# Optimization experiments

Measured on AMD Instinct MI355X. Metric: run time of the kernel, lower is better.

## Reference

```python
import jax, jax.numpy as jnp
import numpy as np


def setup_inputs() -> dict:
    key = jax.random.key(0)
    ks = jax.random.split(key, 7)
    B, C, W, H = 4, 256, 128, 128
    s = 1.0 / np.sqrt(C)
    return {
        "x": jax.random.normal(ks[0], (B, C, W, H), dtype=jnp.float32),
        "wq": jax.random.normal(ks[1], (C, C), dtype=jnp.float32) * s,
        "bq": jax.random.normal(ks[2], (C,), dtype=jnp.float32) * s,
        "wk": jax.random.normal(ks[3], (C, C), dtype=jnp.float32) * s,
        "bk": jax.random.normal(ks[4], (C,), dtype=jnp.float32) * s,
        "wv": jax.random.normal(ks[5], (C, C), dtype=jnp.float32) * s,
        "bv": jax.random.normal(ks[6], (C,), dtype=jnp.float32) * s,
    }


def reference(x, wq, bq, wk, bk, wv, bv):
    B, C, W, H = x.shape
    N = W * H
    xf = x.reshape(B, C, N)  # flatten spatial: (B, C, N)
    # 1x1 convs are channel-mixing GEMMs: out[b,o,n] = sum_c w[o,c] x[b,c,n] + b[o]
    q = jnp.einsum('oc,bcn->bon', wq, xf) + bq[:, None]
    k = jnp.einsum('oc,bcn->bon', wk, xf) + bk[:, None]
    v = jnp.einsum('oc,bcn->bon', wv, xf) + bv[:, None]
    # channel-channel energy: (B, C, C)
    energy = jnp.einsum('bcn,bdn->bcd', q, k) / jnp.sqrt(jnp.float32(N))
    attention = jax.nn.softmax(energy, axis=-1)
    out = jnp.einsum('bcd,bdn->bcn', attention, v)
    return out.reshape(B, C, W, H) + x
```

## Files before the change

kernel.cpp:

```cpp
#include <hip/hip_runtime.h>
#include <stdint.h>

#define BB 4
#define CC 256
#define NN 16384
#define NSL 32

typedef unsigned short u16;
typedef __attribute__((ext_vector_type(8))) __bf16 bf16x8;
typedef __attribute__((ext_vector_type(4))) float f32x4;

__device__ __forceinline__ u16 f2bf(float f) {
  union { float f; uint32_t u; } c;
  c.f = f;
  uint32_t u = c.u;
  return (u16)((u + 0x7fffu + ((u >> 16) & 1u)) >> 16);
}

__device__ __forceinline__ void g2l16(const u16* g, u16* l) {
  __builtin_amdgcn_global_load_lds((__attribute__((address_space(1))) void*)g,
                                   (__attribute__((address_space(3))) void*)l, 16, 0, 0);
}

__device__ __forceinline__ void stage128x32(const u16* src, int stride, u16* lds, int tid) {
  int r = tid >> 2;
  int c = (tid & 3) << 3;
  g2l16(src + (size_t)r * stride + c, lds + r * 32 + c);
  g2l16(src + (size_t)(r + 64) * stride + c, lds + (r + 64) * 32 + c);
}

__device__ __forceinline__ void stage128x32_w8(const u16* src, int stride, u16* lds, int tid) {
  int r = tid >> 2;
  int c = (tid & 3) << 3;
  g2l16(src + (size_t)r * stride + c, lds + r * 32 + c);
}

__device__ __forceinline__ void stage256x32_w8(const u16* src, int stride, u16* lds, int tid) {
  int r = tid >> 2;
  int c = (tid & 3) << 3;
  g2l16(src + (size_t)r * stride + c, lds + r * 32 + c);
  g2l16(src + (size_t)(r + 128) * stride + c, lds + (r + 128) * 32 + c);
}

__device__ __forceinline__ void mfma_tile(const u16* As, const u16* Bs, int mb, int nb,
                                          int l16, int q8, f32x4 acc[4][4]) {
  bf16x8 af[4], bf[4];
#pragma unroll
  for (int i = 0; i < 4; i++) af[i] = *(const bf16x8*)&As[(mb + i * 16 + l16) * 32 + q8];
#pragma unroll
  for (int i = 0; i < 4; i++) bf[i] = *(const bf16x8*)&Bs[(nb + i * 16 + l16) * 32 + q8];
#pragma unroll
  for (int i = 0; i < 4; i++)
#pragma unroll
    for (int j = 0; j < 4; j++)
      acc[i][j] = __builtin_amdgcn_mfma_f32_16x16x32_bf16(af[i], bf[j], acc[i][j], 0, 0, 0);
}

__global__ __launch_bounds__(256) void prep_kernel(const float* __restrict__ x,
                                                   u16* __restrict__ xb,
                                                   u16* __restrict__ xbT,
                                                   float* __restrict__ s_part) {
  __shared__ float t[64][65];
  __shared__ float rs[64][4];
  int n0 = blockIdx.x * 64, c0 = blockIdx.y * 64, bz = blockIdx.z;
  int tid = threadIdx.x;
  int rr0 = tid >> 4, q4 = (tid & 15) * 4;
  const float* xs = x + ((size_t)bz * CC + c0) * NN + n0;
  u16* xbp = xb + ((size_t)bz * CC + c0) * NN + n0;
#pragma unroll
  for (int cc = rr0; cc < 64; cc += 16) {
    float4 v = *(const float4*)&xs[(size_t)cc * NN + q4];
    t[cc][q4] = v.x; t[cc][q4 + 1] = v.y; t[cc][q4 + 2] = v.z; t[cc][q4 + 3] = v.w;
    union { u16 h[4]; uint2 u; } pk;
    pk.h[0] = f2bf(v.x); pk.h[1] = f2bf(v.y); pk.h[2] = f2bf(v.z); pk.h[3] = f2bf(v.w);
    *(uint2*)&xbp[(size_t)cc * NN + q4] = pk.u;
  }
  __syncthreads();
  {
    int r = tid >> 2, q = tid & 3;
    float p = 0.f;
#pragma unroll
    for (int i = 0; i < 16; i++) p += t[r][q * 16 + i];
    rs[r][q] = p;
  }
  u16* od = xbT + ((size_t)bz * NN + n0) * CC + c0;
#pragma unroll
  for (int nn = rr0; nn < 64; nn += 16) {
    union { u16 h[4]; uint2 u; } pk;
    pk.h[0] = f2bf(t[q4][nn]); pk.h[1] = f2bf(t[q4 + 1][nn]);
    pk.h[2] = f2bf(t[q4 + 2][nn]); pk.h[3] = f2bf(t[q4 + 3][nn]);
    *(uint2*)&od[(size_t)nn * CC + q4] = pk.u;
  }
  __syncthreads();
  if (tid < 64)
    s_part[((size_t)bz * 256 + blockIdx.x) * CC + c0 + tid] =
        rs[tid][0] + rs[tid][1] + rs[tid][2] + rs[tid][3];
}

__global__ __launch_bounds__(256) void gram_kernel(const u16* __restrict__ xb,
                                                   float* __restrict__ Gp) {
  __shared__ u16 As[2][128 * 32], Bs[2][128 * 32];
  int tid = threadIdx.x;
  int c0 = (blockIdx.x >> 1) * 128, d0 = (blockIdx.x & 1) * 128;
  int sl = blockIdx.y, bz = blockIdx.z;
  const u16* A = xb + ((size_t)bz * CC + c0) * NN + sl * 512;
  const u16* Bt = xb + ((size_t)bz * CC + d0) * NN + sl * 512;
  f32x4 acc[4][4] = {};
  int wave = tid >> 6, lane = tid & 63;
  int mb = (wave >> 1) * 64, nb = (wave & 1) * 64;
  int quad = lane >> 4, l16 = lane & 15, q8 = quad * 8;
  for (int kk = 0; kk < 512; kk += 64) {
    stage128x32(A + kk, NN, As[0], tid);
    stage128x32(A + kk + 32, NN, As[1], tid);
    stage128x32(Bt + kk, NN, Bs[0], tid);
    stage128x32(Bt + kk + 32, NN, Bs[1], tid);
    __syncthreads();
    mfma_tile(As[0], Bs[0], mb, nb, l16, q8, acc);
    mfma_tile(As[1], Bs[1], mb, nb, l16, q8, acc);
    __syncthreads();
  }
  float* gp = Gp + ((size_t)sl * BB + bz) * CC * CC;
#pragma unroll
  for (int i = 0; i < 4; i++)
#pragma unroll
    for (int j = 0; j < 4; j++)
#pragma unroll
      for (int r = 0; r < 4; r++)
        gp[(size_t)(c0 + mb + i * 16 + quad * 4 + r) * CC + d0 + nb + j * 16 + l16] =
            acc[i][j][r];
}

__global__ __launch_bounds__(256) void reduce_kernel(const float* __restrict__ Gp,
                                                     const float* __restrict__ s_part,
                                                     const float* __restrict__ Wk,
                                                     float* __restrict__ G,
                                                     float* __restrict__ s,
                                                     float* __restrict__ WkT) {
  __shared__ float tw[32][33];
  int t = threadIdx.x, blk = blockIdx.x;
  size_t base = ((size_t)blk * 256 + t) * 4;
  float ax = 0.f, ay = 0.f, az = 0.f, aw = 0.f;
#pragma unroll 8
  for (int sl = 0; sl < NSL; sl++) {
    float4 v = *(const float4*)&Gp[(size_t)sl * (BB * CC * CC) + base];
    ax += v.x; ay += v.y; az += v.z; aw += v.w;
  }
  float4 o; o.x = ax; o.y = ay; o.z = az; o.w = aw;
  *(float4*)&G[base] = o;
  if (blk < BB) {
    float a = 0.f;
#pragma unroll 8
    for (int nt = 0; nt < 256; nt++) a += s_part[((size_t)blk * 256 + nt) * CC + t];
    s[blk * CC + t] = a;
  }
  if (blk < 64) {
    int tr = blk >> 3, tc = blk & 7;
    int r = t >> 5, c = t & 31;
#pragma unroll
    for (int i = 0; i < 4; i++)
      tw[r + i * 8][c] = Wk[(size_t)(tr * 32 + r + i * 8) * CC + tc * 32 + c];
    __syncthreads();
#pragma unroll
    for (int i = 0; i < 4; i++)
      WkT[(size_t)(tc * 32 + r + i * 8) * CC + tr * 32 + c] = tw[c][r + i * 8];
  }
}

__global__ __launch_bounds__(256) void mid_kernel(
    const float* __restrict__ G, const float* __restrict__ s,
    const float* __restrict__ Wq, const float* __restrict__ WkT,
    const float* __restrict__ Wv,
    const float* __restrict__ bq, const float* __restrict__ bk,
    const float* __restrict__ bv,
    u16* __restrict__ Mvb, float* __restrict__ bo) {
  __shared__ float sS[CC];
  __shared__ float rS[2][CC];
  __shared__ float attS[2][CC];
  __shared__ float redA[2][4], redB[2][4], redC[2][4], redD[2][4];
  int t = threadIdx.x;
  int o0 = blockIdx.x * 2, b = blockIdx.y;
  int wv = t >> 6, ln = t & 63;
  sS[t] = s[b * CC + t];
  __syncthreads();
  float p0 = Wq[(size_t)o0 * CC + t] * sS[t];
  float p1 = Wq[(size_t)(o0 + 1) * CC + t] * sS[t];
#pragma unroll
  for (int d = 32; d > 0; d >>= 1) {
    p0 += __shfl_xor(p0, d, 64);
    p1 += __shfl_xor(p1, d, 64);
  }
  if (ln == 0) { redA[0][wv] = p0; redA[1][wv] = p1; }
  __syncthreads();
  float up0 = redA[0][0] + redA[0][1] + redA[0][2] + redA[0][3] + 16384.f * bq[o0];
  float up1 = redA[1][0] + redA[1][1] + redA[1][2] + redA[1][3] + 16384.f * bq[o0 + 1];
  const float* Gb = G + (size_t)b * CC * CC;
  const float* wq0 = Wq + (size_t)o0 * CC;
  const float* wq1 = wq0 + CC;
  float r0 = bq[o0] * sS[t], r1 = bq[o0 + 1] * sS[t];
#pragma unroll 8
  for (int d = 0; d < CC; d++) {
    float g = Gb[d * CC + t];
    r0 += wq0[d] * g;
    r1 += wq1[d] * g;
  }
  rS[0][t] = r0;
  rS[1][t] = r1;
  __syncthreads();
  float e0 = up0 * bk[t], e1 = up1 * bk[t];
#pragma unroll 8
  for (int c = 0; c < CC; c++) {
    float w = WkT[(size_t)c * CC + t];
    e0 += rS[0][c] * w;
    e1 += rS[1][c] * w;
  }
  e0 *= 0.0078125f;
  e1 *= 0.0078125f;
  float m0 = e0, m1 = e1;
#pragma unroll
  for (int d = 32; d > 0; d >>= 1) {
    m0 = fmaxf(m0, __shfl_xor(m0, d, 64));
    m1 = fmaxf(m1, __shfl_xor(m1, d, 64));
  }
  if (ln == 0) { redB[0][wv] = m0; redB[1][wv] = m1; }
  __syncthreads();
  m0 = fmaxf(fmaxf(redB[0][0], redB[0][1]), fmaxf(redB[0][2], redB[0][3]));
  m1 = fmaxf(fmaxf(redB[1][0], redB[1][1]), fmaxf(redB[1][2], redB[1][3]));
  e0 = __expf(e0 - m0);
  e1 = __expf(e1 - m1);
  float s0 = e0, s1 = e1;
#pragma unroll
  for (int d = 32; d > 0; d >>= 1) {
    s0 += __shfl_xor(s0, d, 64);
    s1 += __shfl_xor(s1, d, 64);
  }
  if (ln == 0) { redC[0][wv] = s0; redC[1][wv] = s1; }
  __syncthreads();
  float inv0 = 1.f / (redC[0][0] + redC[0][1] + redC[0][2] + redC[0][3]);
  float inv1 = 1.f / (redC[1][0] + redC[1][1] + redC[1][2] + redC[1][3]);
  float a0 = e0 * inv0, a1 = e1 * inv1;
  attS[0][t] = a0;
  attS[1][t] = a1;
  float b0 = a0 * bv[t], b1 = a1 * bv[t];
#pragma unroll
  for (int d = 32; d > 0; d >>= 1) {
    b0 += __shfl_xor(b0, d, 64);
    b1 += __shfl_xor(b1, d, 64);
  }
  if (ln == 0) { redD[0][wv] = b0; redD[1][wv] = b1; }
  __syncthreads();
  if (t == 0) bo[b * CC + o0] = redD[0][0] + redD[0][1] + redD[0][2] + redD[0][3];
  if (t == 1) bo[b * CC + o0 + 1] = redD[1][0] + redD[1][1] + redD[1][2] + redD[1][3];
  float mv0 = 0.f, mv1 = 0.f;
#pragma unroll 8
  for (int d = 0; d < CC; d++) {
    float w = Wv[d * CC + t];
    mv0 += attS[0][d] * w;
    mv1 += attS[1][d] * w;
  }
  Mvb[((size_t)b * CC + o0) * CC + t] = f2bf(mv0);
  Mvb[((size_t)b * CC + o0 + 1) * CC + t] = f2bf(mv1);
}

__global__ __launch_bounds__(512) void out_kernel(const u16* __restrict__ Mvb,
                                                  const u16* __restrict__ xbT,
                                                  const float* __restrict__ bo,
                                                  const float* __restrict__ x,
                                                  float* __restrict__ out) {
  __shared__ u16 As[2][128 * 32], Bs[2][256 * 32];
  int tid = threadIdx.x;
  int n0 = blockIdx.x * 256, m0 = blockIdx.y * 128, bz = blockIdx.z;
  const u16* A = Mvb + (size_t)bz * CC * CC + (size_t)m0 * CC;
  const u16* Bt = xbT + ((size_t)bz * NN + n0) * CC;
  f32x4 acc[4][4] = {};
  int wave = tid >> 6, lane = tid & 63;
  int mb = (wave & 1) * 64, nb = (wave >> 1) * 64;
  int quad = lane >> 4, l16 = lane & 15, q8 = quad * 8;
  for (int kk = 0; kk < CC; kk += 64) {
    stage128x32_w8(A + kk, CC, As[0], tid);
    stage128x32_w8(A + kk + 32, CC, As[1], tid);
    stage256x32_w8(Bt + kk, CC, Bs[0], tid);
    stage256x32_w8(Bt + kk + 32, CC, Bs[1], tid);
    __syncthreads();
    mfma_tile(As[0], Bs[0], mb, nb, l16, q8, acc);
    mfma_tile(As[1], Bs[1], mb, nb, l16, q8, acc);
    __syncthreads();
  }
#pragma unroll
  for (int i = 0; i < 4; i++)
#pragma unroll
    for (int r = 0; r < 4; r++) {
      int cg = m0 + mb + i * 16 + quad * 4 + r;
      float bc = bo[bz * CC + cg];
#pragma unroll
      for (int j = 0; j < 4; j++) {
        int ng = n0 + nb + j * 16 + l16;
        size_t idx = ((size_t)bz * CC + cg) * NN + ng;
        out[idx] = acc[i][j][r] + bc + x[idx];
      }
    }
}

extern "C" void kernel_launch(void* const* d_in, const int* in_sizes, int n_in,
                              void* d_out, int out_size, void* d_ws, size_t ws_size,
                              hipStream_t stream) {
  (void)in_sizes; (void)n_in; (void)out_size; (void)ws_size;
  const float* x = (const float*)d_in[0];
  const float* wq = (const float*)d_in[1];
  const float* bq = (const float*)d_in[2];
  const float* wk = (const float*)d_in[3];
  const float* bk = (const float*)d_in[4];
  const float* wv = (const float*)d_in[5];
  const float* bv = (const float*)d_in[6];
  float* out = (float*)d_out;

  char* ws = (char*)d_ws;
  u16* xb      = (u16*)(ws + 0);
  u16* xbT     = (u16*)(ws + 33554432);
  float* Gp    = (float*)(ws + 67108864);
  float* G     = (float*)(ws + 100663296);
  float* s_prt = (float*)(ws + 101711872);
  float* s     = (float*)(ws + 102760448);
  u16* Mvb     = (u16*)(ws + 102764544);
  float* bo    = (float*)(ws + 103288832);
  float* WkT   = (float*)(ws + 103292928);

  prep_kernel<<<dim3(NN / 64, CC / 64, BB), 256, 0, stream>>>(x, xb, xbT, s_prt);
  gram_kernel<<<dim3(4, NSL, BB), 256, 0, stream>>>(xb, Gp);
  reduce_kernel<<<256, 256, 0, stream>>>(Gp, s_prt, wk, G, s, WkT);
  mid_kernel<<<dim3(CC / 2, BB), 256, 0, stream>>>(G, s, wq, WkT, wv, bq, bk, bv, Mvb, bo);
  out_kernel<<<dim3(NN / 256, CC / 128, BB), 512, 0, stream>>>(Mvb, xbT, bo, x, out);
}
```

Baseline: 233.6 us.

## Restructure mid_kernel for 4 rows per block and vectorize out_kernel epilogue via LDS

```diff
diff --git a/kernel.cpp b/kernel.cpp
--- a/kernel.cpp
+++ b/kernel.cpp
@@ -166,7 +166,7 @@
   }
 }
 
-__global__ __launch_bounds__(256) void mid_kernel(
+__global__ __launch_bounds__(512) void mid_kernel(
     const float* __restrict__ G, const float* __restrict__ s,
     const float* __restrict__ Wq, const float* __restrict__ WkT,
     const float* __restrict__ Wv,
@@ -174,91 +174,136 @@
     const float* __restrict__ bv,
     u16* __restrict__ Mvb, float* __restrict__ bo) {
   __shared__ float sS[CC];
-  __shared__ float rS[2][CC];
-  __shared__ float attS[2][CC];
-  __shared__ float redA[2][4], redB[2][4], redC[2][4], redD[2][4];
+  __shared__ float wqS[4][CC];
+  __shared__ float rS[4][CC];
+  __shared__ float attS[4][CC];
+  __shared__ float part[4][8][CC];
+  __shared__ float redA[4][4], redB[4][4], redC[4][4], redD[4][4];
   int t = threadIdx.x;
-  int o0 = blockIdx.x * 2, b = blockIdx.y;
+  int o0 = blockIdx.x * 4, b = blockIdx.y;
   int wv = t >> 6, ln = t & 63;
-  sS[t] = s[b * CC + t];
-  __syncthreads();
-  float p0 = Wq[(size_t)o0 * CC + t] * sS[t];
-  float p1 = Wq[(size_t)(o0 + 1) * CC + t] * sS[t];
+  int col = t & 255;
+  int row_a = t >> 8, row_b = row_a + 2;
+  int c4 = ln << 2;
+  int d0 = wv << 5;
+  if (t < CC) sS[t] = s[b * CC + t];
+  {
+    const float* wqsrc = Wq + (size_t)o0 * CC;
+    ((float*)wqS)[t] = wqsrc[t];
+    ((float*)wqS)[t + 512] = wqsrc[t + 512];
+  }
+  __syncthreads();
+  float pa = wqS[row_a][col] * sS[col];
+  float pb = wqS[row_b][col] * sS[col];
 #pragma unroll
   for (int d = 32; d > 0; d >>= 1) {
-    p0 += __shfl_xor(p0, d, 64);
-    p1 += __shfl_xor(p1, d, 64);
-  }
-  if (ln == 0) { redA[0][wv] = p0; redA[1][wv] = p1; }
-  __syncthreads();
-  float up0 = redA[0][0] + redA[0][1] + redA[0][2] + redA[0][3] + 16384.f * bq[o0];
-  float up1 = redA[1][0] + redA[1][1] + redA[1][2] + redA[1][3] + 16384.f * bq[o0 + 1];
+    pa += __shfl_xor(pa, d, 64);
+    pb += __shfl_xor(pb, d, 64);
+  }
+  if (ln == 0) { redA[row_a][wv & 3] = pa; redA[row_b][wv & 3] = pb; }
+  __syncthreads();
+  float up_a = redA[row_a][0] + redA[row_a][1] + redA[row_a][2] + redA[row_a][3] +
+               16384.f * bq[o0 + row_a];
+  float up_b = redA[row_b][0] + redA[row_b][1] + redA[row_b][2] + redA[row_b][3] +
+               16384.f * bq[o0 + row_b];
   const float* Gb = G + (size_t)b * CC * CC;
-  const float* wq0 = Wq + (size_t)o0 * CC;
-  const float* wq1 = wq0 + CC;
-  float r0 = bq[o0] * sS[t], r1 = bq[o0 + 1] * sS[t];
-#pragma unroll 8
-  for (int d = 0; d < CC; d++) {
-    float g = Gb[d * CC + t];
-    r0 += wq0[d] * g;
-    r1 += wq1[d] * g;
-  }
-  rS[0][t] = r0;
-  rS[1][t] = r1;
-  __syncthreads();
-  float e0 = up0 * bk[t], e1 = up1 * bk[t];
-#pragma unroll 8
-  for (int c = 0; c < CC; c++) {
-    float w = WkT[(size_t)c * CC + t];
-    e0 += rS[0][c] * w;
-    e1 += rS[1][c] * w;
-  }
-  e0 *= 0.0078125f;
-  e1 *= 0.0078125f;
-  float m0 = e0, m1 = e1;
+  {
+    f32x4 va[4] = {};
+    const float* gp = Gb + (size_t)d0 * CC + c4;
+#pragma unroll 8
+    for (int i = 0; i < 32; i++) {
+      f32x4 g4 = *(const f32x4*)(gp + (size_t)i * CC);
+      float w0 = wqS[0][d0 + i], w1 = wqS[1][d0 + i];
+      float w2 = wqS[2][d0 + i], w3 = wqS[3][d0 + i];
+      va[0] += g4 * w0; va[1] += g4 * w1; va[2] += g4 * w2; va[3] += g4 * w3;
+    }
+#pragma unroll
+    for (int r = 0; r < 4; r++) *(f32x4*)&part[r][wv][c4] = va[r];
+  }
+  __syncthreads();
+  {
+    float r_a = bq[o0 + row_a] * sS[col];
+    float r_b = bq[o0 + row_b] * sS[col];
+#pragma unroll
+    for (int w = 0; w < 8; w++) { r_a += part[row_a][w][col]; r_b += part[row_b][w][col]; }
+    rS[row_a][col] = r_a;
+    rS[row_b][col] = r_b;
+  }
+  __syncthreads();
+  {
+    f32x4 ve[4] = {};
+    const float* wkp = WkT + (size_t)d0 * CC + c4;
+#pragma unroll 8
+    for (int i = 0; i < 32; i++) {
+      f32x4 w4 = *(const f32x4*)(wkp + (size_t)i * CC);
+      float r0 = rS[0][d0 + i], r1 = rS[1][d0 + i];
+      float r2 = rS[2][d0 + i], r3 = rS[3][d0 + i];
+      ve[0] += w4 * r0; ve[1] += w4 * r1; ve[2] += w4 * r2; ve[3] += w4 * r3;
+    }
+#pragma unroll
+    for (int r = 0; r < 4; r++) *(f32x4*)&part[r][wv][c4] = ve[r];
+  }
+  __syncthreads();
+  float bkc = bk[col];
+  float e_a = up_a * bkc, e_b = up_b * bkc;
+#pragma unroll
+  for (int w = 0; w < 8; w++) { e_a += part[row_a][w][col]; e_b += part[row_b][w][col]; }
+  e_a *= 0.0078125f;
+  e_b *= 0.0078125f;
+  float m_a = e_a, m_b = e_b;
 #pragma unroll
   for (int d = 32; d > 0; d >>= 1) {
-    m0 = fmaxf(m0, __shfl_xor(m0, d, 64));
-    m1 = fmaxf(m1, __shfl_xor(m1, d, 64));
-  }
-  if (ln == 0) { redB[0][wv] = m0; redB[1][wv] = m1; }
-  __syncthreads();
-  m0 = fmaxf(fmaxf(redB[0][0], redB[0][1]), fmaxf(redB[0][2], redB[0][3]));
-  m1 = fmaxf(fmaxf(redB[1][0], redB[1][1]), fmaxf(redB[1][2], redB[1][3]));
-  e0 = __expf(e0 - m0);
-  e1 = __expf(e1 - m1);
-  float s0 = e0, s1 = e1;
+    m_a = fmaxf(m_a, __shfl_xor(m_a, d, 64));
+    m_b = fmaxf(m_b, __shfl_xor(m_b, d, 64));
+  }
+  if (ln == 0) { redB[row_a][wv & 3] = m_a; redB[row_b][wv & 3] = m_b; }
+  __syncthreads();
+  m_a = fmaxf(fmaxf(redB[row_a][0], redB[row_a][1]), fmaxf(redB[row_a][2], redB[row_a][3]));
+  m_b = fmaxf(fmaxf(redB[row_b][0], redB[row_b][1]), fmaxf(redB[row_b][2], redB[row_b][3]));
+  e_a = __expf(e_a - m_a);
+  e_b = __expf(e_b - m_b);
+  float s_a = e_a, s_b = e_b;
 #pragma unroll
   for (int d = 32; d > 0; d >>= 1) {
-    s0 += __shfl_xor(s0, d, 64);
-    s1 += __shfl_xor(s1, d, 64);
-  }
-  if (ln == 0) { redC[0][wv] = s0; redC[1][wv] = s1; }
-  __syncthreads();
-  float inv0 = 1.f / (redC[0][0] + redC[0][1] + redC[0][2] + redC[0][3]);
-  float inv1 = 1.f / (redC[1][0] + redC[1][1] + redC[1][2] + redC[1][3]);
-  float a0 = e0 * inv0, a1 = e1 * inv1;
-  attS[0][t] = a0;
-  attS[1][t] = a1;
-  float b0 = a0 * bv[t], b1 = a1 * bv[t];
+    s_a += __shfl_xor(s_a, d, 64);
+    s_b += __shfl_xor(s_b, d, 64);
+  }
+  if (ln == 0) { redC[row_a][wv & 3] = s_a; redC[row_b][wv & 3] = s_b; }
+  __syncthreads();
+  float inv_a = 1.f / (redC[row_a][0] + redC[row_a][1] + redC[row_a][2] + redC[row_a][3]);
+  float inv_b = 1.f / (redC[row_b][0] + redC[row_b][1] + redC[row_b][2] + redC[row_b][3]);
+  float at_a = e_a * inv_a, at_b = e_b * inv_b;
+  attS[row_a][col] = at_a;
+  attS[row_b][col] = at_b;
+  float bvc = bv[col];
+  float ba = at_a * bvc, bb = at_b * bvc;
 #pragma unroll
   for (int d = 32; d > 0; d >>= 1) {
-    b0 += __shfl_xor(b0, d, 64);
-    b1 += __shfl_xor(b1, d, 64);
-  }
-  if (ln == 0) { redD[0][wv] = b0; redD[1][wv] = b1; }
-  __syncthreads();
-  if (t == 0) bo[b * CC + o0] = redD[0][0] + redD[0][1] + redD[0][2] + redD[0][3];
-  if (t == 1) bo[b * CC + o0 + 1] = redD[1][0] + redD[1][1] + redD[1][2] + redD[1][3];
-  float mv0 = 0.f, mv1 = 0.f;
-#pragma unroll 8
-  for (int d = 0; d < CC; d++) {
-    float w = Wv[d * CC + t];
-    mv0 += attS[0][d] * w;
-    mv1 += attS[1][d] * w;
-  }
-  Mvb[((size_t)b * CC + o0) * CC + t] = f2bf(mv0);
-  Mvb[((size_t)b * CC + o0 + 1) * CC + t] = f2bf(mv1);
+    ba += __shfl_xor(ba, d, 64);
+    bb += __shfl_xor(bb, d, 64);
+  }
+  if (ln == 0) { redD[row_a][wv & 3] = ba; redD[row_b][wv & 3] = bb; }
+  __syncthreads();
+  if (t < 4) bo[b * CC + o0 + t] = redD[t][0] + redD[t][1] + redD[t][2] + redD[t][3];
+  {
+    f32x4 vm[4] = {};
+    const float* wp = Wv + (size_t)d0 * CC + c4;
+#pragma unroll 8
+    for (int i = 0; i < 32; i++) {
+      f32x4 w4 = *(const f32x4*)(wp + (size_t)i * CC);
+      float a0 = attS[0][d0 + i], a1 = attS[1][d0 + i];
+      float a2 = attS[2][d0 + i], a3 = attS[3][d0 + i];
+      vm[0] += w4 * a0; vm[1] += w4 * a1; vm[2] += w4 * a2; vm[3] += w4 * a3;
+    }
+#pragma unroll
+    for (int r = 0; r < 4; r++) *(f32x4*)&part[r][wv][c4] = vm[r];
+  }
+  __syncthreads();
+  float mv_a = 0.f, mv_b = 0.f;
+#pragma unroll
+  for (int w = 0; w < 8; w++) { mv_a += part[row_a][w][col]; mv_b += part[row_b][w][col]; }
+  Mvb[((size_t)b * CC + o0 + row_a) * CC + col] = f2bf(mv_a);
+  Mvb[((size_t)b * CC + o0 + row_b) * CC + col] = f2bf(mv_b);
 }
 
 __global__ __launch_bounds__(512) void out_kernel(const u16* __restrict__ Mvb,
@@ -266,7 +311,10 @@
                                                   const float* __restrict__ bo,
                                                   const float* __restrict__ x,
                                                   float* __restrict__ out) {
-  __shared__ u16 As[2][128 * 32], Bs[2][256 * 32];
+  __shared__ union {
+    struct { u16 As[2][128 * 32]; u16 Bs[2][256 * 32]; } st;
+    float scr[8][64][20];
+  } sm;
   int tid = threadIdx.x;
   int n0 = blockIdx.x * 256, m0 = blockIdx.y * 128, bz = blockIdx.z;
   const u16* A = Mvb + (size_t)bz * CC * CC + (size_t)m0 * CC;
@@ -276,28 +324,43 @@
   int mb = (wave & 1) * 64, nb = (wave >> 1) * 64;
   int quad = lane >> 4, l16 = lane & 15, q8 = quad * 8;
   for (int kk = 0; kk < CC; kk += 64) {
-    stage128x32_w8(A + kk, CC, As[0], tid);
-    stage128x32_w8(A + kk + 32, CC, As[1], tid);
-    stage256x32_w8(Bt + kk, CC, Bs[0], tid);
-    stage256x32_w8(Bt + kk + 32, CC, Bs[1], tid);
-    __syncthreads();
-    mfma_tile(As[0], Bs[0], mb, nb, l16, q8, acc);
-    mfma_tile(As[1], Bs[1], mb, nb, l16, q8, acc);
-    __syncthreads();
-  }
-#pragma unroll
-  for (int i = 0; i < 4; i++)
-#pragma unroll
-    for (int r = 0; r < 4; r++) {
-      int cg = m0 + mb + i * 16 + quad * 4 + r;
-      float bc = bo[bz * CC + cg];
-#pragma unroll
-      for (int j = 0; j < 4; j++) {
-        int ng = n0 + nb + j * 16 + l16;
-        size_t idx = ((size_t)bz * CC + cg) * NN + ng;
-        out[idx] = acc[i][j][r] + bc + x[idx];
-      }
+    stage128x32_w8(A + kk, CC, sm.st.As[0], tid);
+    stage128x32_w8(A + kk + 32, CC, sm.st.As[1], tid);
+    stage256x32_w8(Bt + kk, CC, sm.st.Bs[0], tid);
+    stage256x32_w8(Bt + kk + 32, CC, sm.st.Bs[1], tid);
+    __syncthreads();
+    mfma_tile(sm.st.As[0], sm.st.Bs[0], mb, nb, l16, q8, acc);
+    mfma_tile(sm.st.As[1], sm.st.Bs[1], mb, nb, l16, q8, acc);
+    __syncthreads();
+  }
+  int l4 = lane >> 2;
+  int cgl = lane & 3;
+  float bc[4];
+#pragma unroll
+  for (int kq = 0; kq < 4; kq++) bc[kq] = bo[bz * CC + m0 + mb + kq * 16 + l4];
+#pragma unroll
+  for (int j = 0; j < 4; j++) {
+#pragma unroll
+    for (int i = 0; i < 4; i++)
+#pragma unroll
+      for (int r = 0; r < 4; r++)
+        sm.scr[wave][i * 16 + quad * 4 + r][l16] = acc[i][j][r];
+#pragma unroll
+    for (int kq = 0; kq < 4; kq++) {
+      int rloc = kq * 16 + l4;
+      f32x4 v4 = *(const f32x4*)&sm.scr[wave][rloc][cgl * 4];
+      int cg = m0 + mb + rloc;
+      int ng = n0 + nb + j * 16 + cgl * 4;
+      size_t idx = ((size_t)bz * CC + cg) * NN + ng;
+      float4 xv = *(const float4*)&x[idx];
+      float4 o4;
+      o4.x = v4[0] + bc[kq] + xv.x;
+      o4.y = v4[1] + bc[kq] + xv.y;
+      o4.z = v4[2] + bc[kq] + xv.z;
+      o4.w = v4[3] + bc[kq] + xv.w;
+      *(float4*)&out[idx] = o4;
     }
+  }
 }
 
 extern "C" void kernel_launch(void* const* d_in, const int* in_sizes, int n_in,
@@ -327,6 +390,6 @@
   prep_kernel<<<dim3(NN / 64, CC / 64, BB), 256, 0, stream>>>(x, xb, xbT, s_prt);
   gram_kernel<<<dim3(4, NSL, BB), 256, 0, stream>>>(xb, Gp);
   reduce_kernel<<<256, 256, 0, stream>>>(Gp, s_prt, wk, G, s, WkT);
-  mid_kernel<<<dim3(CC / 2, BB), 256, 0, stream>>>(G, s, wq, WkT, wv, bq, bk, bv, Mvb, bo);
+  mid_kernel<<<dim3(CC / 4, BB), 512, 0, stream>>>(G, s, wq, WkT, wv, bq, bk, bv, Mvb, bo);
   out_kernel<<<dim3(NN / 256, CC / 128, BB), 512, 0, stream>>>(Mvb, xbT, bo, x, out);
 }
```

After: 218.9 us. 1.07x faster.
